# Kernel optimization log

Measured on AMD Instinct MI355X. Metric: run time of the kernel, lower is better.

The kernel has to match this reference:

```python
import jax, jax.numpy as jnp
import numpy as np

K = 10          # neighbors, hard-coded in MLP1.forward
NEG_SLOPE = 0.2 # LeakyReLU slope
EPS = 1e-5      # BatchNorm2d default eps


def setup_inputs() -> dict:
    key = jax.random.key(0)
    k1, k2, k3, k4 = jax.random.split(key, 4)
    B, C, N = 8, 6, 4096
    x = jax.random.normal(k1, (B, C, N), dtype=jnp.float32)
    W = jax.random.normal(k2, (64, 6), dtype=jnp.float32) * 0.2      # conv1x1 weight (O, I)
    gamma = jax.random.uniform(k3, (64,), jnp.float32, 0.5, 1.5)     # BN weight
    beta = jax.random.normal(k4, (64,), dtype=jnp.float32) * 0.1     # BN bias
    return {"x": x, "W": W, "gamma": gamma, "beta": beta}


def _knn_idx(x3, k):
    # pairwise_distance[b,i,j] = -||x_i - x_j||^2 (as in the torch knn)
    inner = jnp.einsum('bdn,bdm->bnm', x3, x3)          # x_i . x_j
    xx = jnp.sum(x3 * x3, axis=1)                       # (B, N)
    pd = 2.0 * inner - xx[:, :, None] - xx[:, None, :]  # (B, N, N)
    _, idx = jax.lax.top_k(pd, k)                       # k nearest (incl. self)
    return idx                                          # (B, N, k) int32


def reference(x, W, gamma, beta):
    # x: (B, 6, N)
    idx = _knn_idx(x[:, :3], K)                          # (B, N, k)
    # gather neighbor features: feat[b,c,n,j] = x[b,c,idx[b,n,j]]
    feat = jax.vmap(lambda xb, ib: xb[:, ib])(x, idx)    # (B, 6, N, k)
    # center xyz over the k neighbors and scale by 10
    xyz = feat[:, :3]
    xyz = (xyz - jnp.mean(xyz, axis=-1, keepdims=True)) * 10.0
    feat = jnp.concatenate([xyz, feat[:, 3:]], axis=1)   # (B, 6, N, k)
    # 1x1 conv (6 -> 64), no bias
    y = jnp.einsum('oc,bcnk->bonk', W, feat)             # (B, 64, N, k)
    # BatchNorm2d in train mode: batch stats over (B, N, k), biased variance
    mu = jnp.mean(y, axis=(0, 2, 3), keepdims=True)
    var = jnp.mean((y - mu) ** 2, axis=(0, 2, 3), keepdims=True)
    y = (y - mu) * jax.lax.rsqrt(var + EPS)
    y = y * gamma[None, :, None, None] + beta[None, :, None, None]
    # LeakyReLU(0.2)
    y = jnp.where(y >= 0, y, NEG_SLOPE * y)
    # max over neighbors k
    y = jnp.max(y, axis=-1)                              # (B, 64, N)
    # global max + mean pooling over N, concat along last axis
    x1 = jnp.max(y, axis=-1)                             # (B, 64)
    x2 = jnp.mean(y, axis=-1)                            # (B, 64)
    return jnp.concatenate([x1, x2], axis=-1)            # (B, 128)
```

## Files before the change

kernel.cpp:

```cpp
#include <hip/hip_runtime.h>
#include <float.h>

#define K_NN 10
#define BATCH 8
#define CIN 6
#define NPTS 4096
#define COUT 64
#define NSEG 8
#define SEGLEN (NPTS / NSEG)
#define CHUNK 16
#define NCHUNK (SEGLEN / CHUNK)
#define NWORD (SEGLEN / 32)
#define NEG_SLOPE 0.2f
#define BN_EPS 1e-5f

static constexpr size_t OFF_IDX  = 0;
static constexpr size_t OFF_PTS  = OFF_IDX + (size_t)BATCH * K_NN * NPTS * sizeof(int);
static constexpr size_t OFF_PTS2 = OFF_PTS + (size_t)BATCH * NPTS * sizeof(float4);
static constexpr size_t OFF_Q    = OFF_PTS2 + (size_t)BATCH * NPTS * sizeof(float4);
static constexpr size_t SZ_Q     = (size_t)NSEG * BATCH * NPTS * K_NN * sizeof(int);
static constexpr size_t OFF_ST   = OFF_Q + SZ_Q;

__device__ __forceinline__ float wave_sum(float v) {
#pragma unroll
    for (int m = 32; m >= 1; m >>= 1) v += __shfl_xor(v, m, 64);
    return v;
}
__device__ __forceinline__ float wave_max(float v) {
#pragma unroll
    for (int m = 32; m >= 1; m >>= 1) v = fmaxf(v, __shfl_xor(v, m, 64));
    return v;
}

__device__ __forceinline__ float distp(float qx, float qy, float qz, float4 c) {
    return fmaf(c.x, qx, fmaf(c.y, qy, fmaf(c.z, qz, -c.w)));
}

__device__ __forceinline__ float fmax3(float a, float b, float c) {
    return fmaxf(fmaxf(a, b), c);
}

#define CHL(cj) { float _hi = fmaxf(cj, t); t = fminf(cj, t); cj = _hi; }

#define CSWP(va, vb, ia, ib) \
    if (va > vb) { float _tv = va; va = vb; vb = _tv; int _ti = ia; ia = ib; ib = _ti; }

#define INSERT10(dd, mm) \
    if ((dd) > v9) { \
        v9 = (dd); i9 = (mm); \
        CSWP(v9, v8, i9, i8) \
        CSWP(v8, v7, i8, i7) \
        CSWP(v7, v6, i7, i6) \
        CSWP(v6, v5, i6, i5) \
        CSWP(v5, v4, i5, i4) \
        CSWP(v4, v3, i4, i3) \
        CSWP(v3, v2, i3, i2) \
        CSWP(v2, v1, i2, i1) \
        CSWP(v1, v0, i1, i0) \
    }

__global__ __launch_bounds__(256) void prep_pts(const float* __restrict__ x,
                                                float4* __restrict__ pts,
                                                float4* __restrict__ pts2,
                                                double* __restrict__ stats) {
    if (blockIdx.x == 0 && threadIdx.x < 27) stats[threadIdx.x] = 0.0;
    int t = blockIdx.x * 256 + threadIdx.x;
    int b = t >> 12;
    int n = t & (NPTS - 1);
    const float* xb = x + (size_t)b * CIN * NPTS;
    float x0 = xb[n];
    float x1 = xb[NPTS + n];
    float x2 = xb[2 * NPTS + n];
    pts[t] = make_float4(2.0f * x0, 2.0f * x1, 2.0f * x2, x0 * x0 + x1 * x1 + x2 * x2);
    float x3 = xb[3 * NPTS + n];
    float x4 = xb[4 * NPTS + n];
    float x5 = xb[5 * NPTS + n];
    pts2[t] = make_float4(x3, x4, x5, 0.0f);
}

__global__ __launch_bounds__(256, 4) void knn_part(const float4* __restrict__ pts,
                                                   int* __restrict__ part) {
    int b = blockIdx.y;
    int s = blockIdx.z;
    int n = blockIdx.x * 256 + threadIdx.x;
    const float4* p = pts + (size_t)b * NPTS;
    float4 q4 = p[n];
    float qx = 0.5f * q4.x, qy = 0.5f * q4.y, qz = 0.5f * q4.z;
    int m0 = s * SEGLEN;

    float c0 = -FLT_MAX, c1 = -FLT_MAX, c2 = -FLT_MAX, c3 = -FLT_MAX, c4 = -FLT_MAX;
    float c5 = -FLT_MAX, c6 = -FLT_MAX, c7 = -FLT_MAX, c8 = -FLT_MAX, c9 = -FLT_MAX;

    for (int ch = 0; ch < NCHUNK; ch++) {
        const float4* cp = p + (m0 + ch * CHUNK);
        float d0  = distp(qx, qy, qz, cp[0]);
        float d1  = distp(qx, qy, qz, cp[1]);
        float d2  = distp(qx, qy, qz, cp[2]);
        float d3  = distp(qx, qy, qz, cp[3]);
        float d4  = distp(qx, qy, qz, cp[4]);
        float d5  = distp(qx, qy, qz, cp[5]);
        float d6  = distp(qx, qy, qz, cp[6]);
        float d7  = distp(qx, qy, qz, cp[7]);
        float d8  = distp(qx, qy, qz, cp[8]);
        float d9  = distp(qx, qy, qz, cp[9]);
        float d10 = distp(qx, qy, qz, cp[10]);
        float d11 = distp(qx, qy, qz, cp[11]);
        float d12 = distp(qx, qy, qz, cp[12]);
        float d13 = distp(qx, qy, qz, cp[13]);
        float d14 = distp(qx, qy, qz, cp[14]);
        float d15 = distp(qx, qy, qz, cp[15]);
        float a0 = fmax3(d0, d1, d2);
        float a1 = fmax3(d3, d4, d5);
        float a2 = fmax3(d6, d7, d8);
        float a3 = fmax3(d9, d10, d11);
        float a4 = fmax3(d12, d13, d14);
        float t = fmaxf(fmax3(fmax3(a0, a1, a2), a3, a4), d15);
        CHL(c0) CHL(c1) CHL(c2) CHL(c3) CHL(c4)
        CHL(c5) CHL(c6) CHL(c7) CHL(c8) CHL(c9)
    }
    float thr = c9;

    float v0 = -FLT_MAX, v1 = -FLT_MAX, v2 = -FLT_MAX, v3 = -FLT_MAX, v4 = -FLT_MAX;
    float v5 = -FLT_MAX, v6 = -FLT_MAX, v7 = -FLT_MAX, v8 = -FLT_MAX, v9 = -FLT_MAX;
    int i0 = 0, i1 = 0, i2 = 0, i3 = 0, i4 = 0;
    int i5 = 0, i6 = 0, i7 = 0, i8 = 0, i9 = 0;

    for (int w = 0; w < NWORD; w++) {
        const float4* cp = p + (m0 + w * 32);
        unsigned int mask = 0u;
#pragma unroll
        for (int u = 0; u < 32; u++) {
            float d = distp(qx, qy, qz, cp[u]);
            mask = (mask << 1) | (d >= thr ? 1u : 0u);
        }
        int base = m0 + w * 32;
        while (mask) {
            int j = __builtin_clz(mask);
            mask ^= (0x80000000u >> j);
            int m = base + j;
            float4 cc = p[m];
            float d = distp(qx, qy, qz, cc);
            INSERT10(d, m)
        }
    }

    int* o = part + (((size_t)s * BATCH + b) * K_NN) * NPTS + n;
    o[(size_t)0 * NPTS] = i0;
    o[(size_t)1 * NPTS] = i1;
    o[(size_t)2 * NPTS] = i2;
    o[(size_t)3 * NPTS] = i3;
    o[(size_t)4 * NPTS] = i4;
    o[(size_t)5 * NPTS] = i5;
    o[(size_t)6 * NPTS] = i6;
    o[(size_t)7 * NPTS] = i7;
    o[(size_t)8 * NPTS] = i8;
    o[(size_t)9 * NPTS] = i9;
}

__global__ __launch_bounds__(512, 8) void merge_kernel(const float4* __restrict__ pts,
                                                       const int* __restrict__ part,
                                                       int* __restrict__ idxo) {
    __shared__ float dml[NSEG][K_NN][64];
    __shared__ unsigned short iml[NSEG][K_NN][64];

    int b  = blockIdx.y;
    int ln = threadIdx.x & 63;
    int wv = threadIdx.x >> 6;
    int wvu = __builtin_amdgcn_readfirstlane(wv);
    int n  = blockIdx.x * 64 + ln;
    const float4* p = pts + (size_t)b * NPTS;
    float4 q4 = p[n];
    float qx = 0.5f * q4.x, qy = 0.5f * q4.y, qz = 0.5f * q4.z;

    float v0 = -FLT_MAX, v1 = -FLT_MAX, v2 = -FLT_MAX, v3 = -FLT_MAX, v4 = -FLT_MAX;
    float v5 = -FLT_MAX, v6 = -FLT_MAX, v7 = -FLT_MAX, v8 = -FLT_MAX, v9 = -FLT_MAX;
    int i0 = 0, i1 = 0, i2 = 0, i3 = 0, i4 = 0;
    int i5 = 0, i6 = 0, i7 = 0, i8 = 0, i9 = 0;

    {
        const int* pp = part + (((size_t)wvu * BATCH + b) * K_NN) * NPTS + n;
#pragma unroll
        for (int j = 0; j < K_NN; j++) {
            int m = pp[(size_t)j * NPTS];
            float4 cc = p[m];
            float d = distp(qx, qy, qz, cc);
            INSERT10(d, m)
        }
    }

    dml[wv][0][ln] = v0; iml[wv][0][ln] = (unsigned short)i0;
    dml[wv][1][ln] = v1; iml[wv][1][ln] = (unsigned short)i1;
    dml[wv][2][ln] = v2; iml[wv][2][ln] = (unsigned short)i2;
    dml[wv][3][ln] = v3; iml[wv][3][ln] = (unsigned short)i3;
    dml[wv][4][ln] = v4; iml[wv][4][ln] = (unsigned short)i4;
    dml[wv][5][ln] = v5; iml[wv][5][ln] = (unsigned short)i5;
    dml[wv][6][ln] = v6; iml[wv][6][ln] = (unsigned short)i6;
    dml[wv][7][ln] = v7; iml[wv][7][ln] = (unsigned short)i7;
    dml[wv][8][ln] = v8; iml[wv][8][ln] = (unsigned short)i8;
    dml[wv][9][ln] = v9; iml[wv][9][ln] = (unsigned short)i9;
    __syncthreads();

    if (wvu == 0) {
        float v0 = -FLT_MAX, v1 = -FLT_MAX, v2 = -FLT_MAX, v3 = -FLT_MAX, v4 = -FLT_MAX;
        float v5 = -FLT_MAX, v6 = -FLT_MAX, v7 = -FLT_MAX, v8 = -FLT_MAX, v9 = -FLT_MAX;
        int i0 = 0, i1 = 0, i2 = 0, i3 = 0, i4 = 0;
        int i5 = 0, i6 = 0, i7 = 0, i8 = 0, i9 = 0;
#pragma unroll
        for (int w = 0; w < NSEG; w++) {
#pragma unroll
            for (int j = 0; j < K_NN; j++) {
                float d = dml[w][j][ln];
                int m = iml[w][j][ln];
                INSERT10(d, m)
            }
        }
        int* o = idxo + (size_t)b * K_NN * NPTS + n;
        o[(size_t)0 * NPTS] = i0;
        o[(size_t)1 * NPTS] = i1;
        o[(size_t)2 * NPTS] = i2;
        o[(size_t)3 * NPTS] = i3;
        o[(size_t)4 * NPTS] = i4;
        o[(size_t)5 * NPTS] = i5;
        o[(size_t)6 * NPTS] = i6;
        o[(size_t)7 * NPTS] = i7;
        o[(size_t)8 * NPTS] = i8;
        o[(size_t)9 * NPTS] = i9;
    }
}

__global__ __launch_bounds__(256) void feat_kernel(const float4* __restrict__ pts,
                                                   const float4* __restrict__ pts2,
                                                   const float* __restrict__ W,
                                                   const int* __restrict__ idx,
                                                   float* __restrict__ q,
                                                   double* __restrict__ stats) {
    __shared__ float sW[COUT * CIN];
    __shared__ float sred[4][27];
    for (int i = threadIdx.x; i < COUT * CIN; i += 256) sW[i] = W[i];
    __syncthreads();

    int b = blockIdx.y;
    int og = blockIdx.z;
    int n = blockIdx.x * 256 + threadIdx.x;
    const float4* p  = pts  + (size_t)b * NPTS;
    const float4* p2 = pts2 + (size_t)b * NPTS;

    int nb[K_NN];
#pragma unroll
    for (int k = 0; k < K_NN; k++) nb[k] = idx[((size_t)b * K_NN + k) * NPTS + n];

    float f[CIN][K_NN];
#pragma unroll
    for (int k = 0; k < K_NN; k++) {
        float4 c = p[nb[k]];
        f[0][k] = 0.5f * c.x; f[1][k] = 0.5f * c.y; f[2][k] = 0.5f * c.z;
    }
#pragma unroll
    for (int k = 0; k < K_NN; k++) {
        float4 c2 = p2[nb[k]];
        f[3][k] = c2.x; f[4][k] = c2.y; f[5][k] = c2.z;
    }

#pragma unroll
    for (int c = 0; c < 3; c++) {
        float s = 0.f;
#pragma unroll
        for (int k = 0; k < K_NN; k++) s += f[c][k];
        float m = s / 10.0f;
#pragma unroll
        for (int k = 0; k < K_NN; k++) f[c][k] = (f[c][k] - m) * 10.0f;
    }

    float* qb = q + (size_t)b * COUT * NPTS + n;
    int o0 = og * 16;
#pragma unroll
    for (int oo = 0; oo < 16; oo++) {
        int o = o0 + oo;
        float w0 = sW[o * 6 + 0], w1 = sW[o * 6 + 1], w2 = sW[o * 6 + 2];
        float w3 = sW[o * 6 + 3], w4 = sW[o * 6 + 4], w5 = sW[o * 6 + 5];
        float mx = -FLT_MAX;
#pragma unroll
        for (int k = 0; k < K_NN; k++) {
            float y = w0 * f[0][k] + w1 * f[1][k] + w2 * f[2][k] +
                      w3 * f[3][k] + w4 * f[4][k] + w5 * f[5][k];
            mx = fmaxf(mx, y);
        }
        qb[(size_t)o * NPTS] = mx;
    }

    if (og != 0) return;

    float s1[CIN];
#pragma unroll
    for (int c = 0; c < CIN; c++) {
        float s = 0.f;
#pragma unroll
        for (int k = 0; k < K_NN; k++) s += f[c][k];
        s1[c] = s;
    }
    float s2[21];
#pragma unroll
    for (int i = 0; i < 21; i++) s2[i] = 0.f;
#pragma unroll
    for (int k = 0; k < K_NN; k++) {
        int pp = 0;
#pragma unroll
        for (int c = 0; c < CIN; c++)
#pragma unroll
            for (int c2 = c; c2 < CIN; c2++) {
                s2[pp] += f[c][k] * f[c2][k];
                pp++;
            }
    }
#pragma unroll
    for (int c = 0; c < CIN; c++) s1[c] = wave_sum(s1[c]);
#pragma unroll
    for (int i = 0; i < 21; i++) s2[i] = wave_sum(s2[i]);

    int wv = threadIdx.x >> 6;
    int ln = threadIdx.x & 63;
    if (ln == 0) {
#pragma unroll
        for (int c = 0; c < CIN; c++) sred[wv][c] = s1[c];
#pragma unroll
        for (int i = 0; i < 21; i++) sred[wv][6 + i] = s2[i];
    }
    __syncthreads();
    if (threadIdx.x < 27) {
        float t = sred[0][threadIdx.x] + sred[1][threadIdx.x] +
                  sred[2][threadIdx.x] + sred[3][threadIdx.x];
        atomicAdd(&stats[threadIdx.x], (double)t);
    }
}

__global__ __launch_bounds__(256) void reduce_kernel(const float* __restrict__ q,
                                                     const double* __restrict__ stats,
                                                     const float* __restrict__ W,
                                                     const float* __restrict__ gamma,
                                                     const float* __restrict__ beta,
                                                     float* __restrict__ out) {
    int o = blockIdx.x;
    int b = blockIdx.y;

    __shared__ float s_sc, s_sh;
    if (threadIdx.x == 0) {
        const double minv = 1.0 / (double)((size_t)BATCH * NPTS * K_NN);
        double w[CIN];
#pragma unroll
        for (int c = 0; c < CIN; c++) w[c] = (double)W[o * CIN + c];
        double mu = 0.0;
#pragma unroll
        for (int c = 0; c < CIN; c++) mu += w[c] * stats[c];
        mu *= minv;
        double ey2 = 0.0;
        int pp = 6;
#pragma unroll
        for (int c = 0; c < CIN; c++)
#pragma unroll
            for (int c2 = c; c2 < CIN; c2++) {
                double v = w[c] * w[c2] * stats[pp];
                ey2 += (c2 == c) ? v : 2.0 * v;
                pp++;
            }
        ey2 *= minv;
        double var = ey2 - mu * mu;
        float scale = gamma[o] * rsqrtf((float)var + BN_EPS);
        float shift = beta[o] - (float)mu * scale;
        s_sc = scale;
        s_sh = shift;
    }
    __syncthreads();
    float scale = s_sc, shift = s_sh;

    const float* qp = q + ((size_t)b * COUT + o) * NPTS;
    float mx = -FLT_MAX, sm = 0.f;
    for (int i = threadIdx.x; i < NPTS; i += 256) {
        float z = scale * qp[i] + shift;
        z = (z >= 0.f) ? z : NEG_SLOPE * z;
        mx = fmaxf(mx, z);
        sm += z;
    }
    mx = wave_max(mx);
    sm = wave_sum(sm);
    __shared__ float smx[4], ssm2[4];
    int wv = threadIdx.x >> 6;
    int ln = threadIdx.x & 63;
    if (ln == 0) { smx[wv] = mx; ssm2[wv] = sm; }
    __syncthreads();
    if (threadIdx.x == 0) {
        float m = fmaxf(fmaxf(smx[0], smx[1]), fmaxf(smx[2], smx[3]));
        float s = ssm2[0] + ssm2[1] + ssm2[2] + ssm2[3];
        out[b * 2 * COUT + o] = m;
        out[b * 2 * COUT + COUT + o] = s * (1.0f / (float)NPTS);
    }
}

extern "C" void kernel_launch(void* const* d_in, const int* in_sizes, int n_in,
                              void* d_out, int out_size, void* d_ws, size_t ws_size,
                              hipStream_t stream) {
    const float* x     = (const float*)d_in[0];
    const float* W     = (const float*)d_in[1];
    const float* gamma = (const float*)d_in[2];
    const float* beta  = (const float*)d_in[3];
    float* out = (float*)d_out;

    char* ws = (char*)d_ws;
    int*    idx   = (int*)(ws + OFF_IDX);
    float4* pts   = (float4*)(ws + OFF_PTS);
    float4* pts2  = (float4*)(ws + OFF_PTS2);
    int*    part  = (int*)(ws + OFF_Q);
    float*  q     = (float*)(ws + OFF_Q);
    double* stats = (double*)(ws + OFF_ST);

    prep_pts<<<BATCH * NPTS / 256, 256, 0, stream>>>(x, pts, pts2, stats);
    knn_part<<<dim3(NPTS / 256, BATCH, NSEG), 256, 0, stream>>>(pts, part);
    merge_kernel<<<dim3(NPTS / 64, BATCH), 512, 0, stream>>>(pts, part, idx);
    feat_kernel<<<dim3(NPTS / 256, BATCH, 4), 256, 0, stream>>>(pts, pts2, W, idx, q, stats);
    reduce_kernel<<<dim3(COUT, BATCH), 256, 0, stream>>>(q, stats, W, gamma, beta, out);
}
```

Baseline: 182.5 us.

## Fuse kNN partial search, merge and feature conv into one kernel

Merges the per-segment kNN search, the cross-segment top-k merge and the feature/conv/stats stage into a single kernel. Each of the 8 waves in a block scans one segment for the same 64 query points, wave 0 merges the candidates, and the final indices go to LDS instead of global memory. All waves then compute 8 output channels each. This removes two kernel launches and the global round trips for the partial and final index arrays. In exchange the block shape is fixed at 64 queries per block, wave 0 does the serial merge while the other waves wait, and the occupancy hint drops from 8 to 4.

```diff
diff --git a/kernel.cpp b/kernel.cpp
--- a/kernel.cpp
+++ b/kernel.cpp
@@ -14,12 +14,10 @@
 #define NEG_SLOPE 0.2f
 #define BN_EPS 1e-5f
 
-static constexpr size_t OFF_IDX  = 0;
-static constexpr size_t OFF_PTS  = OFF_IDX + (size_t)BATCH * K_NN * NPTS * sizeof(int);
+static constexpr size_t OFF_PTS  = 0;
 static constexpr size_t OFF_PTS2 = OFF_PTS + (size_t)BATCH * NPTS * sizeof(float4);
 static constexpr size_t OFF_Q    = OFF_PTS2 + (size_t)BATCH * NPTS * sizeof(float4);
-static constexpr size_t SZ_Q     = (size_t)NSEG * BATCH * NPTS * K_NN * sizeof(int);
-static constexpr size_t OFF_ST   = OFF_Q + SZ_Q;
+static constexpr size_t OFF_ST   = OFF_Q + (size_t)BATCH * COUT * NPTS * sizeof(float);
 
 __device__ __forceinline__ float wave_sum(float v) {
 #pragma unroll
@@ -78,90 +76,18 @@
     pts2[t] = make_float4(x3, x4, x5, 0.0f);
 }
 
-__global__ __launch_bounds__(256, 4) void knn_part(const float4* __restrict__ pts,
-                                                   int* __restrict__ part) {
-    int b = blockIdx.y;
-    int s = blockIdx.z;
-    int n = blockIdx.x * 256 + threadIdx.x;
-    const float4* p = pts + (size_t)b * NPTS;
-    float4 q4 = p[n];
-    float qx = 0.5f * q4.x, qy = 0.5f * q4.y, qz = 0.5f * q4.z;
-    int m0 = s * SEGLEN;
-
-    float c0 = -FLT_MAX, c1 = -FLT_MAX, c2 = -FLT_MAX, c3 = -FLT_MAX, c4 = -FLT_MAX;
-    float c5 = -FLT_MAX, c6 = -FLT_MAX, c7 = -FLT_MAX, c8 = -FLT_MAX, c9 = -FLT_MAX;
-
-    for (int ch = 0; ch < NCHUNK; ch++) {
-        const float4* cp = p + (m0 + ch * CHUNK);
-        float d0  = distp(qx, qy, qz, cp[0]);
-        float d1  = distp(qx, qy, qz, cp[1]);
-        float d2  = distp(qx, qy, qz, cp[2]);
-        float d3  = distp(qx, qy, qz, cp[3]);
-        float d4  = distp(qx, qy, qz, cp[4]);
-        float d5  = distp(qx, qy, qz, cp[5]);
-        float d6  = distp(qx, qy, qz, cp[6]);
-        float d7  = distp(qx, qy, qz, cp[7]);
-        float d8  = distp(qx, qy, qz, cp[8]);
-        float d9  = distp(qx, qy, qz, cp[9]);
-        float d10 = distp(qx, qy, qz, cp[10]);
-        float d11 = distp(qx, qy, qz, cp[11]);
-        float d12 = distp(qx, qy, qz, cp[12]);
-        float d13 = distp(qx, qy, qz, cp[13]);
-        float d14 = distp(qx, qy, qz, cp[14]);
-        float d15 = distp(qx, qy, qz, cp[15]);
-        float a0 = fmax3(d0, d1, d2);
-        float a1 = fmax3(d3, d4, d5);
-        float a2 = fmax3(d6, d7, d8);
-        float a3 = fmax3(d9, d10, d11);
-        float a4 = fmax3(d12, d13, d14);
-        float t = fmaxf(fmax3(fmax3(a0, a1, a2), a3, a4), d15);
-        CHL(c0) CHL(c1) CHL(c2) CHL(c3) CHL(c4)
-        CHL(c5) CHL(c6) CHL(c7) CHL(c8) CHL(c9)
-    }
-    float thr = c9;
-
-    float v0 = -FLT_MAX, v1 = -FLT_MAX, v2 = -FLT_MAX, v3 = -FLT_MAX, v4 = -FLT_MAX;
-    float v5 = -FLT_MAX, v6 = -FLT_MAX, v7 = -FLT_MAX, v8 = -FLT_MAX, v9 = -FLT_MAX;
-    int i0 = 0, i1 = 0, i2 = 0, i3 = 0, i4 = 0;
-    int i5 = 0, i6 = 0, i7 = 0, i8 = 0, i9 = 0;
-
-    for (int w = 0; w < NWORD; w++) {
-        const float4* cp = p + (m0 + w * 32);
-        unsigned int mask = 0u;
-#pragma unroll
-        for (int u = 0; u < 32; u++) {
-            float d = distp(qx, qy, qz, cp[u]);
-            mask = (mask << 1) | (d >= thr ? 1u : 0u);
-        }
-        int base = m0 + w * 32;
-        while (mask) {
-            int j = __builtin_clz(mask);
-            mask ^= (0x80000000u >> j);
-            int m = base + j;
-            float4 cc = p[m];
-            float d = distp(qx, qy, qz, cc);
-            INSERT10(d, m)
-        }
-    }
-
-    int* o = part + (((size_t)s * BATCH + b) * K_NN) * NPTS + n;
-    o[(size_t)0 * NPTS] = i0;
-    o[(size_t)1 * NPTS] = i1;
-    o[(size_t)2 * NPTS] = i2;
-    o[(size_t)3 * NPTS] = i3;
-    o[(size_t)4 * NPTS] = i4;
-    o[(size_t)5 * NPTS] = i5;
-    o[(size_t)6 * NPTS] = i6;
-    o[(size_t)7 * NPTS] = i7;
-    o[(size_t)8 * NPTS] = i8;
-    o[(size_t)9 * NPTS] = i9;
-}
-
-__global__ __launch_bounds__(512, 8) void merge_kernel(const float4* __restrict__ pts,
-                                                       const int* __restrict__ part,
-                                                       int* __restrict__ idxo) {
+__global__ __launch_bounds__(512, 4) void knnmf_kernel(const float4* __restrict__ pts,
+                                                       const float4* __restrict__ pts2,
+                                                       const float* __restrict__ W,
+                                                       float* __restrict__ q,
+                                                       double* __restrict__ stats) {
     __shared__ float dml[NSEG][K_NN][64];
     __shared__ unsigned short iml[NSEG][K_NN][64];
+    __shared__ unsigned short idxL[K_NN][64];
+    __shared__ float sW[COUT * CIN];
+    __shared__ float sstat[27];
+
+    for (int i = threadIdx.x; i < COUT * CIN; i += 512) sW[i] = W[i];
 
     int b  = blockIdx.y;
     int ln = threadIdx.x & 63;
@@ -171,33 +97,76 @@
     const float4* p = pts + (size_t)b * NPTS;
     float4 q4 = p[n];
     float qx = 0.5f * q4.x, qy = 0.5f * q4.y, qz = 0.5f * q4.z;
-
-    float v0 = -FLT_MAX, v1 = -FLT_MAX, v2 = -FLT_MAX, v3 = -FLT_MAX, v4 = -FLT_MAX;
-    float v5 = -FLT_MAX, v6 = -FLT_MAX, v7 = -FLT_MAX, v8 = -FLT_MAX, v9 = -FLT_MAX;
-    int i0 = 0, i1 = 0, i2 = 0, i3 = 0, i4 = 0;
-    int i5 = 0, i6 = 0, i7 = 0, i8 = 0, i9 = 0;
+    int m0 = wvu * SEGLEN;
 
     {
-        const int* pp = part + (((size_t)wvu * BATCH + b) * K_NN) * NPTS + n;
-#pragma unroll
-        for (int j = 0; j < K_NN; j++) {
-            int m = pp[(size_t)j * NPTS];
-            float4 cc = p[m];
-            float d = distp(qx, qy, qz, cc);
-            INSERT10(d, m)
-        }
-    }
-
-    dml[wv][0][ln] = v0; iml[wv][0][ln] = (unsigned short)i0;
-    dml[wv][1][ln] = v1; iml[wv][1][ln] = (unsigned short)i1;
-    dml[wv][2][ln] = v2; iml[wv][2][ln] = (unsigned short)i2;
-    dml[wv][3][ln] = v3; iml[wv][3][ln] = (unsigned short)i3;
-    dml[wv][4][ln] = v4; iml[wv][4][ln] = (unsigned short)i4;
-    dml[wv][5][ln] = v5; iml[wv][5][ln] = (unsigned short)i5;
-    dml[wv][6][ln] = v6; iml[wv][6][ln] = (unsigned short)i6;
-    dml[wv][7][ln] = v7; iml[wv][7][ln] = (unsigned short)i7;
-    dml[wv][8][ln] = v8; iml[wv][8][ln] = (unsigned short)i8;
-    dml[wv][9][ln] = v9; iml[wv][9][ln] = (unsigned short)i9;
+        float c0 = -FLT_MAX, c1 = -FLT_MAX, c2 = -FLT_MAX, c3 = -FLT_MAX, c4 = -FLT_MAX;
+        float c5 = -FLT_MAX, c6 = -FLT_MAX, c7 = -FLT_MAX, c8 = -FLT_MAX, c9 = -FLT_MAX;
+
+        for (int ch = 0; ch < NCHUNK; ch++) {
+            const float4* cp = p + (m0 + ch * CHUNK);
+            float d0  = distp(qx, qy, qz, cp[0]);
+            float d1  = distp(qx, qy, qz, cp[1]);
+            float d2  = distp(qx, qy, qz, cp[2]);
+            float d3  = distp(qx, qy, qz, cp[3]);
+            float d4  = distp(qx, qy, qz, cp[4]);
+            float d5  = distp(qx, qy, qz, cp[5]);
+            float d6  = distp(qx, qy, qz, cp[6]);
+            float d7  = distp(qx, qy, qz, cp[7]);
+            float d8  = distp(qx, qy, qz, cp[8]);
+            float d9  = distp(qx, qy, qz, cp[9]);
+            float d10 = distp(qx, qy, qz, cp[10]);
+            float d11 = distp(qx, qy, qz, cp[11]);
+            float d12 = distp(qx, qy, qz, cp[12]);
+            float d13 = distp(qx, qy, qz, cp[13]);
+            float d14 = distp(qx, qy, qz, cp[14]);
+            float d15 = distp(qx, qy, qz, cp[15]);
+            float a0 = fmax3(d0, d1, d2);
+            float a1 = fmax3(d3, d4, d5);
+            float a2 = fmax3(d6, d7, d8);
+            float a3 = fmax3(d9, d10, d11);
+            float a4 = fmax3(d12, d13, d14);
+            float t = fmaxf(fmax3(fmax3(a0, a1, a2), a3, a4), d15);
+            CHL(c0) CHL(c1) CHL(c2) CHL(c3) CHL(c4)
+            CHL(c5) CHL(c6) CHL(c7) CHL(c8) CHL(c9)
+        }
+        float thr = c9;
+
+        float v0 = -FLT_MAX, v1 = -FLT_MAX, v2 = -FLT_MAX, v3 = -FLT_MAX, v4 = -FLT_MAX;
+        float v5 = -FLT_MAX, v6 = -FLT_MAX, v7 = -FLT_MAX, v8 = -FLT_MAX, v9 = -FLT_MAX;
+        int i0 = 0, i1 = 0, i2 = 0, i3 = 0, i4 = 0;
+        int i5 = 0, i6 = 0, i7 = 0, i8 = 0, i9 = 0;
+
+        for (int w = 0; w < NWORD; w++) {
+            const float4* cp = p + (m0 + w * 32);
+            unsigned int mask = 0u;
+#pragma unroll
+            for (int u = 0; u < 32; u++) {
+                float d = distp(qx, qy, qz, cp[u]);
+                mask = (mask << 1) | (d >= thr ? 1u : 0u);
+            }
+            int base = m0 + w * 32;
+            while (mask) {
+                int j = __builtin_clz(mask);
+                mask ^= (0x80000000u >> j);
+                int m = base + j;
+                float4 cc = p[m];
+                float d = distp(qx, qy, qz, cc);
+                INSERT10(d, m)
+            }
+        }
+
+        dml[wv][0][ln] = v0; iml[wv][0][ln] = (unsigned short)i0;
+        dml[wv][1][ln] = v1; iml[wv][1][ln] = (unsigned short)i1;
+        dml[wv][2][ln] = v2; iml[wv][2][ln] = (unsigned short)i2;
+        dml[wv][3][ln] = v3; iml[wv][3][ln] = (unsigned short)i3;
+        dml[wv][4][ln] = v4; iml[wv][4][ln] = (unsigned short)i4;
+        dml[wv][5][ln] = v5; iml[wv][5][ln] = (unsigned short)i5;
+        dml[wv][6][ln] = v6; iml[wv][6][ln] = (unsigned short)i6;
+        dml[wv][7][ln] = v7; iml[wv][7][ln] = (unsigned short)i7;
+        dml[wv][8][ln] = v8; iml[wv][8][ln] = (unsigned short)i8;
+        dml[wv][9][ln] = v9; iml[wv][9][ln] = (unsigned short)i9;
+    }
     __syncthreads();
 
     if (wvu == 0) {
@@ -214,40 +183,24 @@
                 INSERT10(d, m)
             }
         }
-        int* o = idxo + (size_t)b * K_NN * NPTS + n;
-        o[(size_t)0 * NPTS] = i0;
-        o[(size_t)1 * NPTS] = i1;
-        o[(size_t)2 * NPTS] = i2;
-        o[(size_t)3 * NPTS] = i3;
-        o[(size_t)4 * NPTS] = i4;
-        o[(size_t)5 * NPTS] = i5;
-        o[(size_t)6 * NPTS] = i6;
-        o[(size_t)7 * NPTS] = i7;
-        o[(size_t)8 * NPTS] = i8;
-        o[(size_t)9 * NPTS] = i9;
-    }
-}
-
-__global__ __launch_bounds__(256) void feat_kernel(const float4* __restrict__ pts,
-                                                   const float4* __restrict__ pts2,
-                                                   const float* __restrict__ W,
-                                                   const int* __restrict__ idx,
-                                                   float* __restrict__ q,
-                                                   double* __restrict__ stats) {
-    __shared__ float sW[COUT * CIN];
-    __shared__ float sred[4][27];
-    for (int i = threadIdx.x; i < COUT * CIN; i += 256) sW[i] = W[i];
+        idxL[0][ln] = (unsigned short)i0;
+        idxL[1][ln] = (unsigned short)i1;
+        idxL[2][ln] = (unsigned short)i2;
+        idxL[3][ln] = (unsigned short)i3;
+        idxL[4][ln] = (unsigned short)i4;
+        idxL[5][ln] = (unsigned short)i5;
+        idxL[6][ln] = (unsigned short)i6;
+        idxL[7][ln] = (unsigned short)i7;
+        idxL[8][ln] = (unsigned short)i8;
+        idxL[9][ln] = (unsigned short)i9;
+    }
     __syncthreads();
 
-    int b = blockIdx.y;
-    int og = blockIdx.z;
-    int n = blockIdx.x * 256 + threadIdx.x;
-    const float4* p  = pts  + (size_t)b * NPTS;
     const float4* p2 = pts2 + (size_t)b * NPTS;
 
     int nb[K_NN];
 #pragma unroll
-    for (int k = 0; k < K_NN; k++) nb[k] = idx[((size_t)b * K_NN + k) * NPTS + n];
+    for (int k = 0; k < K_NN; k++) nb[k] = idxL[k][ln];
 
     float f[CIN][K_NN];
 #pragma unroll
@@ -272,9 +225,9 @@
     }
 
     float* qb = q + (size_t)b * COUT * NPTS + n;
-    int o0 = og * 16;
-#pragma unroll
-    for (int oo = 0; oo < 16; oo++) {
+    int o0 = wvu * 8;
+#pragma unroll
+    for (int oo = 0; oo < 8; oo++) {
         int o = o0 + oo;
         float w0 = sW[o * 6 + 0], w1 = sW[o * 6 + 1], w2 = sW[o * 6 + 2];
         float w3 = sW[o * 6 + 3], w4 = sW[o * 6 + 4], w5 = sW[o * 6 + 5];
@@ -288,48 +241,41 @@
         qb[(size_t)o * NPTS] = mx;
     }
 
-    if (og != 0) return;
-
-    float s1[CIN];
-#pragma unroll
-    for (int c = 0; c < CIN; c++) {
-        float s = 0.f;
-#pragma unroll
-        for (int k = 0; k < K_NN; k++) s += f[c][k];
-        s1[c] = s;
-    }
-    float s2[21];
-#pragma unroll
-    for (int i = 0; i < 21; i++) s2[i] = 0.f;
-#pragma unroll
-    for (int k = 0; k < K_NN; k++) {
-        int pp = 0;
-#pragma unroll
-        for (int c = 0; c < CIN; c++)
-#pragma unroll
-            for (int c2 = c; c2 < CIN; c2++) {
-                s2[pp] += f[c][k] * f[c2][k];
-                pp++;
-            }
-    }
-#pragma unroll
-    for (int c = 0; c < CIN; c++) s1[c] = wave_sum(s1[c]);
-#pragma unroll
-    for (int i = 0; i < 21; i++) s2[i] = wave_sum(s2[i]);
-
-    int wv = threadIdx.x >> 6;
-    int ln = threadIdx.x & 63;
-    if (ln == 0) {
-#pragma unroll
-        for (int c = 0; c < CIN; c++) sred[wv][c] = s1[c];
-#pragma unroll
-        for (int i = 0; i < 21; i++) sred[wv][6 + i] = s2[i];
-    }
-    __syncthreads();
-    if (threadIdx.x < 27) {
-        float t = sred[0][threadIdx.x] + sred[1][threadIdx.x] +
-                  sred[2][threadIdx.x] + sred[3][threadIdx.x];
-        atomicAdd(&stats[threadIdx.x], (double)t);
+    if (wvu == 0) {
+        float s1[CIN];
+#pragma unroll
+        for (int c = 0; c < CIN; c++) {
+            float s = 0.f;
+#pragma unroll
+            for (int k = 0; k < K_NN; k++) s += f[c][k];
+            s1[c] = s;
+        }
+        float s2[21];
+#pragma unroll
+        for (int i = 0; i < 21; i++) s2[i] = 0.f;
+#pragma unroll
+        for (int k = 0; k < K_NN; k++) {
+            int pp = 0;
+#pragma unroll
+            for (int c = 0; c < CIN; c++)
+#pragma unroll
+                for (int c2 = c; c2 < CIN; c2++) {
+                    s2[pp] += f[c][k] * f[c2][k];
+                    pp++;
+                }
+        }
+#pragma unroll
+        for (int c = 0; c < CIN; c++) s1[c] = wave_sum(s1[c]);
+#pragma unroll
+        for (int i = 0; i < 21; i++) s2[i] = wave_sum(s2[i]);
+
+        if (ln == 0) {
+#pragma unroll
+            for (int c = 0; c < CIN; c++) sstat[c] = s1[c];
+#pragma unroll
+            for (int i = 0; i < 21; i++) sstat[6 + i] = s2[i];
+        }
+        if (ln < 27) atomicAdd(&stats[ln], (double)sstat[ln]);
     }
 }
 
@@ -405,16 +351,12 @@
     float* out = (float*)d_out;
 
     char* ws = (char*)d_ws;
-    int*    idx   = (int*)(ws + OFF_IDX);
     float4* pts   = (float4*)(ws + OFF_PTS);
     float4* pts2  = (float4*)(ws + OFF_PTS2);
-    int*    part  = (int*)(ws + OFF_Q);
     float*  q     = (float*)(ws + OFF_Q);
     double* stats = (double*)(ws + OFF_ST);
 
     prep_pts<<<BATCH * NPTS / 256, 256, 0, stream>>>(x, pts, pts2, stats);
-    knn_part<<<dim3(NPTS / 256, BATCH, NSEG), 256, 0, stream>>>(pts, part);
-    merge_kernel<<<dim3(NPTS / 64, BATCH), 512, 0, stream>>>(pts, part, idx);
-    feat_kernel<<<dim3(NPTS / 256, BATCH, 4), 256, 0, stream>>>(pts, pts2, W, idx, q, stats);
+    knnmf_kernel<<<dim3(NPTS / 64, BATCH), 512, 0, stream>>>(pts, pts2, W, q, stats);
     reduce_kernel<<<dim3(COUT, BATCH), 256, 0, stream>>>(q, stats, W, gamma, beta, out);
 }
```

New measurement: 165.7 us. 9.2% less time.
